# Optimization experiments

Hardware: AMD Instinct MI355X
Metric: run time of the kernel (lower is better)

## Reference

```python
import jax, jax.numpy as jnp
import numpy as np

N = 50000      # nodes
E = 800000     # edges (before self-loops)
DIN = 2        # dim_input
DEMB = 128     # dim_embedding
H = 8          # n_heads
DV = 16        # dim_values (H*DV == DEMB)
DH = 512       # dim_hidden
L = 2          # n_att_layers
K = 10         # APPNP steps
ALPHA = 0.1
EPS = 1e-5     # BatchNorm eps
NEG_SLOPE = 0.2  # GAT leaky_relu slope


def setup_inputs() -> dict:
    key = jax.random.key(0)
    ks = jax.random.split(key, 16)
    s = 0.05
    inp = {}
    inp["x"] = jax.random.normal(ks[0], (N, DIN), jnp.float32)
    inp["J"] = jax.random.uniform(ks[1], (N, 1), jnp.float32)
    inp["edge_index"] = jax.random.randint(ks[2], (2, E), 0, N, jnp.int32)
    # Lin1: Linear(dim_input+1, dim_embedding)
    inp["lin0_w"] = jax.random.normal(ks[3], (DIN + 1, DEMB), jnp.float32) * s
    inp["lin0_b"] = jnp.zeros((DEMB,), jnp.float32)
    # Per attention layer (stacked over L):
    inp["gat_w"]   = jax.random.normal(ks[4], (L, DEMB, H * DV), jnp.float32) * s
    inp["att_src"] = jax.random.normal(ks[5], (L, H, DV), jnp.float32) * s
    inp["att_dst"] = jax.random.normal(ks[6], (L, H, DV), jnp.float32) * s
    inp["lin1_w"]  = jax.random.normal(ks[7], (L, DV, DEMB), jnp.float32) * s
    inp["bn1_g"]   = jnp.ones((L, DEMB), jnp.float32)
    inp["bn1_b"]   = jnp.zeros((L, DEMB), jnp.float32)
    inp["lin2_w"]  = jax.random.normal(ks[8], (L, DEMB, DH), jnp.float32) * s
    inp["lin2_b"]  = jnp.zeros((L, DH), jnp.float32)
    inp["lin3_w"]  = jax.random.normal(ks[9], (L, DH, DEMB), jnp.float32) * s
    inp["lin3_b"]  = jnp.zeros((L, DEMB), jnp.float32)
    inp["bn2_g"]   = jnp.ones((L, DEMB), jnp.float32)
    inp["bn2_b"]   = jnp.zeros((L, DEMB), jnp.float32)
    return inp


def _bn(z, g, b):
    # BatchNorm1d over nodes, training-mode batch statistics (biased var)
    mu = z.mean(0)
    var = jnp.mean((z - mu) ** 2, axis=0)
    return g * (z - mu) * jax.lax.rsqrt(var + EPS) + b


def reference(x, J, edge_index, lin0_w, lin0_b, gat_w, att_src, att_dst,
              lin1_w, bn1_g, bn1_b, lin2_w, lin2_b, lin3_w, lin3_b,
              bn2_g, bn2_b):
    # add self-loops (PyG GATConv and APPNP defaults)
    loop = jnp.arange(N, dtype=edge_index.dtype)
    src = jnp.concatenate([edge_index[0], loop])  # message source j
    dst = jnp.concatenate([edge_index[1], loop])  # message target i

    h = jnp.concatenate([x, J], axis=1) @ lin0_w + lin0_b  # [N, DEMB]

    for l in range(L):
        # ---- GATConv ----
        xl = (h @ gat_w[l]).reshape(N, H, DV)                # [N,H,DV]
        a_s = (xl * att_src[l]).sum(-1)                      # [N,H]
        a_d = (xl * att_dst[l]).sum(-1)                      # [N,H]
        e = jax.nn.leaky_relu(a_s[src] + a_d[dst], NEG_SLOPE)  # [E',H]
        e = e - jax.ops.segment_max(e, dst, num_segments=N)[dst]
        ee = jnp.exp(e)
        alpha = ee / jax.ops.segment_sum(ee, dst, num_segments=N)[dst]
        msg = xl[src] * alpha[:, :, None]                    # [E',H,DV]
        gat_out = jax.ops.segment_sum(msg, dst, num_segments=N)  # [N,H,DV]
        # lin1 per head then sum over heads
        hsum = jnp.einsum('nhc,cd->nd', gat_out, lin1_w[l])  # [N,DEMB]
        h1 = _bn(h + hsum, bn1_g[l], bn1_b[l])
        h2 = jax.nn.relu(h1 @ lin2_w[l] + lin2_b[l]) @ lin3_w[l] + lin3_b[l]
        h = _bn(h2 + h1, bn2_g[l], bn2_b[l])

    # ---- APPNP: K steps of (1-a)*Ahat h + a*h0, Ahat = D^-1/2 (A+I) D^-1/2 ----
    deg = jax.ops.segment_sum(jnp.ones_like(dst, jnp.float32), dst, num_segments=N)
    dinv = jax.lax.rsqrt(jnp.maximum(deg, 1.0))  # self-loops guarantee deg>=1
    norm = (dinv[src] * dinv[dst])[:, None]      # [E',1]
    h0 = h

    def step(hk, _):
        agg = jax.ops.segment_sum(norm * hk[src], dst, num_segments=N)
        return (1.0 - ALPHA) * agg + ALPHA * h0, None

    h, _ = jax.lax.scan(step, h, None, length=K)
    return jnp.concatenate([h, J], axis=1)  # [N, DEMB+1]
```

## Files before the change

kernel.cpp:

```cpp
#include <hip/hip_runtime.h>

#define NN 50000
#define NP 50048
#define NMT64 782
#define NE 800000
#define EP (NE + NN)
#define DEMB 128
#define DHID 512
#define NB_SCAN 196

typedef unsigned short ushort_t;
typedef __attribute__((ext_vector_type(8))) short short8_t;
typedef __attribute__((ext_vector_type(4))) float float4_t;

__device__ __forceinline__ float bf2f(ushort_t u) {
    return __uint_as_float(((unsigned int)u) << 16);
}
__device__ __forceinline__ ushort_t f2bf(float f) {
    unsigned int x = __float_as_uint(f);
    x += 0x7fffu + ((x >> 16) & 1u);
    return (ushort_t)(x >> 16);
}
__device__ __forceinline__ float lo16(unsigned int w) { return __uint_as_float(w << 16); }
__device__ __forceinline__ float hi16(unsigned int w) { return __uint_as_float(w & 0xffff0000u); }
__device__ __forceinline__ unsigned int pack2(float a, float b) {
    return (unsigned int)f2bf(a) | ((unsigned int)f2bf(b) << 16);
}
__device__ __forceinline__ void gl_lds16(const ushort_t* g, ushort_t* l) {
    __builtin_amdgcn_global_load_lds(
        (const __attribute__((address_space(1))) void*)g,
        (__attribute__((address_space(3))) void*)l, 16, 0, 0);
}
static inline int cdiv(int a, int b) { return (a + b - 1) / b; }

__global__ void k_detect(const unsigned int* __restrict__ Jw, int* __restrict__ flag) {
    if (threadIdx.x != 0 || blockIdx.x != 0) return;
    int votes = 0;
    for (int i = 0; i < 8; ++i) {
        unsigned int w = Jw[i];
        unsigned int ex = (w >> 23) & 0xFFu;
        if ((w >> 31) == 0u && ex >= 100u && ex <= 126u) votes++;
    }
    *flag = (votes >= 6) ? 1 : 0;
}

struct CvtArgs {
    const void* src[16];
    float* dst[16];
    int n[16];
};
__global__ void k_cvt_all(CvtArgs a, const int* __restrict__ flag) {
    int which = blockIdx.y;
    int i = blockIdx.x * 256 + threadIdx.x;
    if (i >= a.n[which]) return;
    float v;
    if (*flag) v = ((const float*)a.src[which])[i];
    else       v = bf2f(((const ushort_t*)a.src[which])[i]);
    a.dst[which][i] = v;
}

struct TrArgs {
    const float* src[6];
    ushort_t* dst[6];
    int K[6];
    int Nc[6];
    int perm[6];
};
__global__ void k_tr_all(TrArgs a) {
    int which = blockIdx.y;
    int idx = blockIdx.x * 256 + threadIdx.x;
    int K = a.K[which], Nc = a.Nc[which];
    if (idx >= K * Nc) return;
    int k = idx / Nc, n = idx - k * Nc;
    int kd = k;
    if (a.perm[which]) {
        int kk = k & 63;
        int ks = kk >> 5, k5 = kk & 31;
        int u = (k5 >> 4) & 1, q = (k5 >> 2) & 3, tt = k5 & 3;
        kd = (k & ~63) | (ks * 32 + q * 8 + tt * 2 + u);
    }
    a.dst[which][n * K + kd] = f2bf(a.src[which][idx]);
}

__global__ void k_deg(const int* __restrict__ ei, int* __restrict__ deg) {
    int e = blockIdx.x * 256 + threadIdx.x;
    if (e >= EP) return;
    int d = (e < NE) ? ei[NE + e] : (e - NE);
    atomicAdd(&deg[d], 1);
}

__global__ void k_part(const int* __restrict__ deg, int* __restrict__ part) {
    __shared__ int sm[256];
    int i = blockIdx.x * 256 + threadIdx.x;
    int v = (i < NN) ? deg[i] : 0;
    sm[threadIdx.x] = v;
    __syncthreads();
    for (int off = 128; off > 0; off >>= 1) {
        if (threadIdx.x < off) sm[threadIdx.x] += sm[threadIdx.x + off];
        __syncthreads();
    }
    if (threadIdx.x == 0) part[blockIdx.x] = sm[0];
}

__global__ void k_scan2(const int* __restrict__ part, int* __restrict__ poff,
                        int* __restrict__ rowp) {
    __shared__ int sm[256];
    int t = threadIdx.x;
    int v = (t < NB_SCAN) ? part[t] : 0;
    sm[t] = v;
    __syncthreads();
    int incl = v;
    for (int off = 1; off < 256; off <<= 1) {
        int u = (t >= off) ? sm[t - off] : 0;
        __syncthreads();
        incl += u;
        sm[t] = incl;
        __syncthreads();
    }
    if (t < NB_SCAN) poff[t] = incl - v;
    if (t == 255) rowp[NN] = sm[255];
}

__global__ void k_rowp(const int* __restrict__ deg, const int* __restrict__ poff,
                       int* __restrict__ rowp, float* __restrict__ dinv,
                       int* __restrict__ fill) {
    __shared__ int sm[256];
    int i = blockIdx.x * 256 + threadIdx.x;
    int t = threadIdx.x;
    int v = (i < NN) ? deg[i] : 0;
    sm[t] = v;
    __syncthreads();
    int incl = v;
    for (int off = 1; off < 256; off <<= 1) {
        int u = (t >= off) ? sm[t - off] : 0;
        __syncthreads();
        incl += u;
        sm[t] = incl;
        __syncthreads();
    }
    if (i < NN) {
        int rp = poff[blockIdx.x] + incl - v;
        rowp[i] = rp;
        fill[i] = rp;
        dinv[i] = rsqrtf(fmaxf((float)v, 1.0f));
    }
}

__global__ void k_fill(const int* __restrict__ ei, int* __restrict__ fillpos,
                       ushort_t* __restrict__ col) {
    int e = blockIdx.x * 256 + threadIdx.x;
    if (e >= EP) return;
    int s, d;
    if (e < NE) { s = ei[e]; d = ei[NE + e]; } else { s = d = e - NE; }
    int pos = atomicAdd(&fillpos[d], 1);
    col[pos] = (ushort_t)s;
}

__global__ void k_lin0(const float* __restrict__ x, const float* __restrict__ J,
                       const float* __restrict__ w, const float* __restrict__ b,
                       ushort_t* __restrict__ hB) {
    int idx = blockIdx.x * 256 + threadIdx.x;
    if (idx >= NN * DEMB) return;
    int n = idx >> 7, d = idx & 127;
    float v = x[n * 2] * w[d] + x[n * 2 + 1] * w[DEMB + d] + J[n] * w[2 * DEMB + d] + b[d];
    hB[idx] = f2bf(v);
}

__global__ void k_att(const unsigned int* __restrict__ xlB, const float* __restrict__ asrc,
                      const float* __restrict__ adst, float* __restrict__ a_s,
                      float* __restrict__ a_d) {
    int idx = blockIdx.x * 256 + threadIdx.x;
    if (idx >= NN * 8) return;
    int n = idx >> 3, hh = idx & 7;
    const unsigned int* row = xlB + (size_t)n * 64 + hh * 8;
    float s = 0.f, d = 0.f;
#pragma unroll
    for (int c = 0; c < 8; ++c) {
        unsigned int w = row[c];
        float v0 = lo16(w), v1 = hi16(w);
        s += v0 * asrc[hh * 16 + 2 * c] + v1 * asrc[hh * 16 + 2 * c + 1];
        d += v0 * adst[hh * 16 + 2 * c] + v1 * adst[hh * 16 + 2 * c + 1];
    }
    a_s[idx] = s;
    a_d[idx] = d;
}

__global__ __launch_bounds__(256) void k_z1s(const ushort_t* __restrict__ hB,
                                             const float* __restrict__ g,
                                             const float* __restrict__ w1,
                                             float* __restrict__ stats) {
    int d = threadIdx.x & 127;
    int rstart = blockIdx.x * 2 + (threadIdx.x >> 7);
    int stride = gridDim.x * 2;
    float s1 = 0.f, s2 = 0.f;
    for (int r = rstart; r < NN; r += stride) {
        const float* gr = g + r * 16;
        float s = bf2f(hB[(size_t)r * DEMB + d]);
#pragma unroll
        for (int c = 0; c < 16; ++c) s += gr[c] * w1[c * DEMB + d];
        s1 += s;
        s2 += s * s;
    }
    __shared__ float b1[256], b2[256];
    b1[threadIdx.x] = s1;
    b2[threadIdx.x] = s2;
    __syncthreads();
    if (threadIdx.x < 128) {
        atomicAdd(&stats[threadIdx.x], b1[threadIdx.x] + b1[threadIdx.x + 128]);
        atomicAdd(&stats[128 + threadIdx.x], b2[threadIdx.x] + b2[threadIdx.x + 128]);
    }
}

__global__ void k_bnapply1(const ushort_t* __restrict__ hB, const float* __restrict__ g,
                           const float* __restrict__ w1, const float* __restrict__ stats,
                           const float* __restrict__ gam, const float* __restrict__ bet,
                           ushort_t* __restrict__ outB) {
    int idx = blockIdx.x * 256 + threadIdx.x;
    if (idx >= NN * DEMB) return;
    int n = idx >> 7, d = idx & 127;
    float s = bf2f(hB[idx]);
    const float* gr = g + n * 16;
#pragma unroll
    for (int c = 0; c < 16; ++c) s += gr[c] * w1[c * DEMB + d];
    const float invN = 1.0f / (float)NN;
    float mu = stats[d] * invN;
    float var = stats[128 + d] * invN - mu * mu;
    float rs = rsqrtf(fmaxf(var, 0.f) + 1e-5f);
    float v = gam[d] * (s - mu) * rs + bet[d];
    outB[idx] = f2bf(v);
}

__global__ void k_bnapply(const ushort_t* __restrict__ zB, const float* __restrict__ stats,
                          const float* __restrict__ gam, const float* __restrict__ bet,
                          ushort_t* __restrict__ outB) {
    int idx = blockIdx.x * 256 + threadIdx.x;
    if (idx >= NN * DEMB) return;
    int d = idx & 127;
    const float invN = 1.0f / (float)NN;
    float mu = stats[d] * invN;
    float var = stats[128 + d] * invN - mu * mu;
    float rs = rsqrtf(fmaxf(var, 0.f) + 1e-5f);
    float v = gam[d] * (bf2f(zB[idx]) - mu) * rs + bet[d];
    outB[idx] = f2bf(v);
}

__global__ void k_bnapply_fin(const unsigned int* __restrict__ zB, const float* __restrict__ stats,
                              const float* __restrict__ gam, const float* __restrict__ bet,
                              const float* __restrict__ dinv,
                              unsigned int* __restrict__ hs, unsigned int* __restrict__ h0p) {
    int idx = blockIdx.x * 256 + threadIdx.x;
    if (idx >= NN * 64) return;
    int n = idx >> 6, d0 = (idx & 63) * 2;
    const float invN = 1.0f / (float)NN;
    unsigned int zw = zB[idx];
    float z0 = lo16(zw), z1 = hi16(zw);
    float mu0 = stats[d0] * invN, mu1 = stats[d0 + 1] * invN;
    float v0 = stats[128 + d0] * invN - mu0 * mu0;
    float v1 = stats[128 + d0 + 1] * invN - mu1 * mu1;
    float rs0 = rsqrtf(fmaxf(v0, 0.f) + 1e-5f);
    float rs1 = rsqrtf(fmaxf(v1, 0.f) + 1e-5f);
    float a = gam[d0] * (z0 - mu0) * rs0 + bet[d0];
    float b = gam[d0 + 1] * (z1 - mu1) * rs1 + bet[d0 + 1];
    float di = dinv[n];
    hs[idx] = pack2(di * a, di * b);
    h0p[idx] = pack2(a, b);
}

__global__ __launch_bounds__(256) void k_gat(const int* __restrict__ rowp,
                                             const ushort_t* __restrict__ col,
                                             const float* __restrict__ a_s, const float* __restrict__ a_d,
                                             const unsigned int* __restrict__ xlB, float* __restrict__ g) {
    int wid = (blockIdx.x * 256 + threadIdx.x) >> 6;
    int lane = threadIdx.x & 63;
    if (wid >= NN) return;
    int p0 = rowp[wid], p1 = rowp[wid + 1];
    int hh = lane >> 3;
    float ad2 = a_d[wid * 8 + hh];
    float acc0 = 0.f, acc1 = 0.f, s = 0.f;
    int p = p0;
    while (p < p1) {
        int cnt = p1 - p;
        if (cnt > 64) cnt = 64;
        int pl = p + lane;
        int jv = (int)col[pl < p1 ? pl : (p1 - 1)];
        int i = 0;
        for (; i + 8 <= cnt; i += 8) {
            int j0 = __shfl(jv, i),     j1 = __shfl(jv, i + 1);
            int j2 = __shfl(jv, i + 2), j3 = __shfl(jv, i + 3);
            int j4 = __shfl(jv, i + 4), j5 = __shfl(jv, i + 5);
            int j6 = __shfl(jv, i + 6), j7 = __shfl(jv, i + 7);
            float e0 = a_s[j0 * 8 + hh] + ad2, e1 = a_s[j1 * 8 + hh] + ad2;
            float e2 = a_s[j2 * 8 + hh] + ad2, e3 = a_s[j3 * 8 + hh] + ad2;
            float e4 = a_s[j4 * 8 + hh] + ad2, e5 = a_s[j5 * 8 + hh] + ad2;
            float e6 = a_s[j6 * 8 + hh] + ad2, e7 = a_s[j7 * 8 + hh] + ad2;
            unsigned int w0 = xlB[j0 * 64 + lane], w1 = xlB[j1 * 64 + lane];
            unsigned int w2 = xlB[j2 * 64 + lane], w3 = xlB[j3 * 64 + lane];
            unsigned int w4 = xlB[j4 * 64 + lane], w5 = xlB[j5 * 64 + lane];
            unsigned int w6 = xlB[j6 * 64 + lane], w7 = xlB[j7 * 64 + lane];
            e0 = e0 > 0.f ? e0 : 0.2f * e0;  e1 = e1 > 0.f ? e1 : 0.2f * e1;
            e2 = e2 > 0.f ? e2 : 0.2f * e2;  e3 = e3 > 0.f ? e3 : 0.2f * e3;
            e4 = e4 > 0.f ? e4 : 0.2f * e4;  e5 = e5 > 0.f ? e5 : 0.2f * e5;
            e6 = e6 > 0.f ? e6 : 0.2f * e6;  e7 = e7 > 0.f ? e7 : 0.2f * e7;
            float al0 = __expf(e0), al1 = __expf(e1), al2 = __expf(e2), al3 = __expf(e3);
            float al4 = __expf(e4), al5 = __expf(e5), al6 = __expf(e6), al7 = __expf(e7);
            s += al0 + al1 + al2 + al3 + al4 + al5 + al6 + al7;
            acc0 += al0 * lo16(w0) + al1 * lo16(w1) + al2 * lo16(w2) + al3 * lo16(w3) +
                    al4 * lo16(w4) + al5 * lo16(w5) + al6 * lo16(w6) + al7 * lo16(w7);
            acc1 += al0 * hi16(w0) + al1 * hi16(w1) + al2 * hi16(w2) + al3 * hi16(w3) +
                    al4 * hi16(w4) + al5 * hi16(w5) + al6 * hi16(w6) + al7 * hi16(w7);
        }
        for (; i < cnt; ++i) {
            int j = __shfl(jv, i);
            float e = a_s[j * 8 + hh] + ad2;
            e = e > 0.f ? e : 0.2f * e;
            float al = __expf(e);
            unsigned int w = xlB[j * 64 + lane];
            s += al;
            acc0 += al * lo16(w);
            acc1 += al * hi16(w);
        }
        p += cnt;
    }
    float inv = 1.f / s;
    acc0 *= inv;
    acc1 *= inv;
    acc0 += __shfl_xor(acc0, 8);  acc1 += __shfl_xor(acc1, 8);
    acc0 += __shfl_xor(acc0, 16); acc1 += __shfl_xor(acc1, 16);
    acc0 += __shfl_xor(acc0, 32); acc1 += __shfl_xor(acc1, 32);
    if (lane < 8) ((float2*)g)[wid * 8 + lane] = make_float2(acc0, acc1);
}

__global__ __launch_bounds__(256) void k_appnp(const int* __restrict__ rowp,
                                               const ushort_t* __restrict__ col,
                                               const float* __restrict__ dinv,
                                               const unsigned int* __restrict__ hs,
                                               const unsigned int* __restrict__ h0p,
                                               unsigned int* __restrict__ hs_out,
                                               const float* __restrict__ Jf,
                                               const int* __restrict__ flag,
                                               void* __restrict__ out, int writeOut) {
    int wid = (blockIdx.x * 256 + threadIdx.x) >> 6;
    int lane = threadIdx.x & 63;
    if (wid >= NN) return;
    int p0 = rowp[wid], p1 = rowp[wid + 1];
    float di = dinv[wid];
    unsigned int hw = h0p[(size_t)wid * 64 + lane];
    float a0 = 0.f, a1 = 0.f;
    int p = p0;
    while (p < p1) {
        int cnt = p1 - p;
        if (cnt > 64) cnt = 64;
        int pl = p + lane;
        int jv = (int)col[pl < p1 ? pl : (p1 - 1)];
        int i = 0;
        for (; i + 8 <= cnt; i += 8) {
            int j0 = __shfl(jv, i),     j1 = __shfl(jv, i + 1);
            int j2 = __shfl(jv, i + 2), j3 = __shfl(jv, i + 3);
            int j4 = __shfl(jv, i + 4), j5 = __shfl(jv, i + 5);
            int j6 = __shfl(jv, i + 6), j7 = __shfl(jv, i + 7);
            unsigned int w0 = hs[j0 * 64 + lane], w1 = hs[j1 * 64 + lane];
            unsigned int w2 = hs[j2 * 64 + lane], w3 = hs[j3 * 64 + lane];
            unsigned int w4 = hs[j4 * 64 + lane], w5 = hs[j5 * 64 + lane];
            unsigned int w6 = hs[j6 * 64 + lane], w7 = hs[j7 * 64 + lane];
            a0 += lo16(w0) + lo16(w1) + lo16(w2) + lo16(w3) +
                  lo16(w4) + lo16(w5) + lo16(w6) + lo16(w7);
            a1 += hi16(w0) + hi16(w1) + hi16(w2) + hi16(w3) +
                  hi16(w4) + hi16(w5) + hi16(w6) + hi16(w7);
        }
        for (; i < cnt; ++i) {
            int j = __shfl(jv, i);
            unsigned int w = hs[j * 64 + lane];
            a0 += lo16(w);
            a1 += hi16(w);
        }
        p += cnt;
    }
    float n0 = 0.9f * di * a0 + 0.1f * lo16(hw);
    float n1 = 0.9f * di * a1 + 0.1f * hi16(hw);
    if (!writeOut) {
        hs_out[(size_t)wid * 64 + lane] = pack2(di * n0, di * n1);
    } else {
        size_t base = (size_t)wid * 129;
        if (*flag) {
            float* o = (float*)out;
            o[base + 2 * lane] = n0;
            o[base + 2 * lane + 1] = n1;
            if (lane == 0) o[base + 128] = Jf[wid];
        } else {
            ushort_t* o = (ushort_t*)out;
            o[base + 2 * lane] = f2bf(n0);
            o[base + 2 * lane + 1] = f2bf(n1);
            if (lane == 0) o[base + 128] = f2bf(Jf[wid]);
        }
    }
}

template <int MODE>
__global__ __launch_bounds__(256) void k_gemm64(const ushort_t* __restrict__ A,
                                                const ushort_t* __restrict__ Bt,
                                                int M, int K, int Nc,
                                                const float* __restrict__ bias,
                                                const ushort_t* __restrict__ res,
                                                ushort_t* __restrict__ outB,
                                                float* __restrict__ stats) {
    __shared__ __align__(16) ushort_t lsA[2][64 * 32];
    __shared__ __align__(16) ushort_t lsB[2][128 * 32];
    int t = threadIdx.x;
    int m0 = blockIdx.x * 64;
    int n0 = blockIdx.y * 128;
    int w = t >> 6, lane = t & 63;
    int row16 = lane & 15, quad = lane >> 4;
    int nbase = w * 32;
    float4_t acc[8];
#pragma unroll
    for (int i = 0; i < 8; ++i) acc[i] = (float4_t){0.f, 0.f, 0.f, 0.f};
    int lrow = lane >> 2;
    int lcol = (lane & 3) * 8;
    const ushort_t* gA  = A  + (size_t)(m0 + w * 16 + lrow) * K + lcol;
    const ushort_t* gB0 = Bt + (size_t)(n0 + w * 32 + lrow) * K + lcol;
    const ushort_t* gB1 = Bt + (size_t)(n0 + w * 32 + 16 + lrow) * K + lcol;
    ushort_t* dA  = &lsA[0][0] + (w * 16) * 32;
    ushort_t* dB0 = &lsB[0][0] + (w * 32) * 32;
    ushort_t* dB1 = &lsB[0][0] + (w * 32 + 16) * 32;
    const int bufStrideA = 64 * 32, bufStrideB = 128 * 32;
    const int nK = K >> 5;
    gl_lds16(gA, dA);
    gl_lds16(gB0, dB0);
    gl_lds16(gB1, dB1);
    for (int kb = 0; kb < nK; ++kb) {
        __syncthreads();
        int nb = kb + 1;
        if (nb < nK) {
            int b = nb & 1;
            int k0 = nb << 5;
            gl_lds16(gA + k0, dA + b * bufStrideA);
            gl_lds16(gB0 + k0, dB0 + b * bufStrideB);
            gl_lds16(gB1 + k0, dB1 + b * bufStrideB);
        }
        const ushort_t* la = &lsA[kb & 1][0];
        const ushort_t* lb = &lsB[kb & 1][0];
        short8_t afr[4], bfr[2];
#pragma unroll
        for (int i = 0; i < 4; ++i)
            afr[i] = *(const short8_t*)(la + (i * 16 + row16) * 32 + quad * 8);
#pragma unroll
        for (int i = 0; i < 2; ++i)
            bfr[i] = *(const short8_t*)(lb + (nbase + i * 16 + row16) * 32 + quad * 8);
#pragma unroll
        for (int mt = 0; mt < 4; ++mt)
#pragma unroll
            for (int nt = 0; nt < 2; ++nt)
                acc[mt * 2 + nt] = __builtin_amdgcn_mfma_f32_16x16x32_bf16(
                    afr[mt], bfr[nt], acc[mt * 2 + nt], 0, 0, 0);
    }
#pragma unroll
    for (int mt = 0; mt < 4; ++mt) {
#pragma unroll
        for (int nt = 0; nt < 2; ++nt) {
            int cc = n0 + nbase + nt * 16 + row16;
#pragma unroll
            for (int r = 0; r < 4; ++r) {
                int rr = m0 + mt * 16 + quad * 4 + r;
                if (rr < M) {
                    outB[(size_t)rr * Nc + cc] = f2bf(acc[mt * 2 + nt][r]);
                }
            }
        }
    }
}

__global__ __launch_bounds__(256, 2) void k_ffn(const ushort_t* __restrict__ A,
                                                const ushort_t* __restrict__ W2t,
                                                const ushort_t* __restrict__ W3t,
                                                const float* __restrict__ b2,
                                                const float* __restrict__ b3,
                                                const ushort_t* __restrict__ res,
                                                ushort_t* __restrict__ outB,
                                                float* __restrict__ stats) {
    __shared__ __align__(16) ushort_t sW2[2][4 * 64 * 32];
    __shared__ __align__(16) ushort_t sW3[2][2 * 128 * 32];
    __shared__ __align__(16) ushort_t sAH[4][2048];
    int t = threadIdx.x;
    int w = t >> 6, lane = t & 63;
    int m0 = blockIdx.x * 64;
    int row16 = lane & 15, quad = lane >> 4;
    int sw = (row16 >> 2) & 3;
    int srow = lane >> 2;
    int klin = lane & 3;

#pragma unroll
    for (int i = 0; i < 4; ++i) {
        int row = i * 16 + srow;
        int kc = klin ^ ((row >> 2) & 3);
        gl_lds16(A + (size_t)(m0 + row) * 128 + w * 32 + kc * 8,
                 &sAH[0][0] + w * 2048 + i * 512);
    }
#pragma unroll
    for (int i = 0; i < 4; ++i) {
        int n = i * 16 + srow;
        int kc = klin ^ ((n >> 2) & 3);
        gl_lds16(W2t + (size_t)n * 128 + w * 32 + kc * 8,
                 &sW2[0][0] + w * 2048 + i * 512);
    }
#pragma unroll
    for (int i = 0; i < 4; ++i) {
        int f = w * 4 + i;
        int ks = f >> 3;
        int n = (f & 7) * 16 + srow;
        int kc = klin ^ ((n >> 2) & 3);
        gl_lds16(W3t + (size_t)n * 512 + ks * 32 + kc * 8,
                 &sW3[0][0] + f * 512);
    }
    __syncthreads();

    short8_t afrA[4];
#pragma unroll
    for (int kb = 0; kb < 4; ++kb)
        afrA[kb] = *(const short8_t*)(&sAH[0][0] + kb * 2048 + (w * 16 + row16) * 32 + (quad ^ sw) * 8);
    __syncthreads();

    float* s1 = (float*)&sAH[0][1024];
    float* s2 = s1 + 128;
    if (t < 128) { s1[t] = 0.f; s2[t] = 0.f; }
    ushort_t* Hbase = &sAH[w][0];

    float4_t accz[8];
#pragma unroll
    for (int i = 0; i < 8; ++i) accz[i] = (float4_t){0.f, 0.f, 0.f, 0.f};

    for (int c = 0; c < 8; ++c) {
        int cb = c & 1;
        if (c < 7) {
            int nb = cb ^ 1;
#pragma unroll
            for (int i = 0; i < 4; ++i) {
                int n = i * 16 + srow;
                int kc = klin ^ ((n >> 2) & 3);
                gl_lds16(W2t + (size_t)((c + 1) * 64 + n) * 128 + w * 32 + kc * 8,
                         &sW2[nb][0] + w * 2048 + i * 512);
            }
#pragma unroll
            for (int i = 0; i < 4; ++i) {
                int f = w * 4 + i;
                int ks = f >> 3;
                int n = (f & 7) * 16 + srow;
                int kc = klin ^ ((n >> 2) & 3);
                gl_lds16(W3t + (size_t)n * 512 + (c + 1) * 64 + ks * 32 + kc * 8,
                         &sW3[nb][0] + f * 512);
            }
        }
        float4_t acch[4];
#pragma unroll
        for (int i = 0; i < 4; ++i) acch[i] = (float4_t){0.f, 0.f, 0.f, 0.f};
#pragma unroll
        for (int kb = 0; kb < 4; ++kb) {
            short8_t bfr[4];
#pragma unroll
            for (int nt = 0; nt < 4; ++nt)
                bfr[nt] = *(const short8_t*)(&sW2[cb][0] + kb * 2048 + (nt * 16 + row16) * 32 + (quad ^ sw) * 8);
#pragma unroll
            for (int nt = 0; nt < 4; ++nt)
                acch[nt] = __builtin_amdgcn_mfma_f32_16x16x32_bf16(afrA[kb], bfr[nt],
                                                                   acch[nt], 0, 0, 0);
        }
        {
            float b2v[4];
#pragma unroll
            for (int nt = 0; nt < 4; ++nt) b2v[nt] = b2[c * 64 + nt * 16 + row16];
#pragma unroll
            for (int r = 0; r < 4; ++r) {
                int row = quad * 4 + r;
                float v0 = acch[0][r] + b2v[0]; v0 = v0 > 0.f ? v0 : 0.f;
                float v1 = acch[1][r] + b2v[1]; v1 = v1 > 0.f ? v1 : 0.f;
                float v2 = acch[2][r] + b2v[2]; v2 = v2 > 0.f ? v2 : 0.f;
                float v3 = acch[3][r] + b2v[3]; v3 = v3 > 0.f ? v3 : 0.f;
                int byteA = row * 128 + ((((row16 >> 2) ^ (row & 7))) << 4) + (row16 & 3) * 4;
                *(unsigned int*)((char*)Hbase + byteA) = pack2(v0, v1);
                *(unsigned int*)((char*)Hbase + (byteA ^ 64)) = pack2(v2, v3);
            }
        }
#pragma unroll
        for (int ks = 0; ks < 2; ++ks) {
            short8_t afrH = *(const short8_t*)((char*)Hbase + row16 * 128 +
                                               ((((ks << 2) | quad) ^ (row16 & 7)) << 4));
            short8_t bfr[8];
#pragma unroll
            for (int nt = 0; nt < 8; ++nt)
                bfr[nt] = *(const short8_t*)(&sW3[cb][0] + ks * 4096 + (nt * 16 + row16) * 32 + (quad ^ sw) * 8);
#pragma unroll
            for (int nt = 0; nt < 8; ++nt)
                accz[nt] = __builtin_amdgcn_mfma_f32_16x16x32_bf16(afrH, bfr[nt],
                                                                   accz[nt], 0, 0, 0);
        }
        __syncthreads();
    }

#pragma unroll
    for (int nt = 0; nt < 8; ++nt) {
        int cc = nt * 16 + row16;
        float bv = b3[cc];
        float ls = 0.f, lq = 0.f;
#pragma unroll
        for (int r = 0; r < 4; ++r) {
            int rr = m0 + w * 16 + quad * 4 + r;
            if (rr < NN) {
                float v = accz[nt][r] + bv + bf2f(res[(size_t)rr * 128 + cc]);
                outB[(size_t)rr * 128 + cc] = f2bf(v);
                ls += v;
                lq += v * v;
            }
        }
        atomicAdd(&s1[cc], ls);
        atomicAdd(&s2[cc], lq);
    }
    __syncthreads();
    if (t < 128) {
        atomicAdd(&stats[t], s1[t]);
        atomicAdd(&stats[128 + t], s2[t]);
    }
}

extern "C" void kernel_launch(void* const* d_in, const int* in_sizes, int n_in,
                              void* d_out, int out_size, void* d_ws, size_t ws_size,
                              hipStream_t stream) {
    const int* ei = (const int*)d_in[2];

    char* p = (char*)d_ws;
    auto alloc = [&](size_t bytes) {
        void* r = (void*)p;
        p += (bytes + 255) & ~(size_t)255;
        return r;
    };
    ushort_t* hB    = (ushort_t*)alloc((size_t)NP * DEMB * 2);
    ushort_t* h1B   = (ushort_t*)alloc((size_t)NP * DEMB * 2);
    ushort_t* xlB   = (ushort_t*)alloc((size_t)NN * DEMB * 2);
    unsigned int* hsA  = (unsigned int*)alloc((size_t)NN * 64 * 4);
    unsigned int* hsB_ = (unsigned int*)alloc((size_t)NN * 64 * 4);
    unsigned int* h0p  = (unsigned int*)alloc((size_t)NN * 64 * 4);
    float*    asv   = (float*)alloc((size_t)NN * 8 * 4);
    float*    adv   = (float*)alloc((size_t)NN * 8 * 4);
    float*    gv    = (float*)alloc((size_t)NN * 16 * 4);
    float*    dinvv = (float*)alloc((size_t)NN * 4);
    float*    stats = (float*)alloc(4 * 256 * 4);
    int*      deg   = (int*)alloc((size_t)NN * 4);
    int*      rowp  = (int*)alloc((size_t)(NN + 1) * 4);
    int*      fill  = (int*)alloc((size_t)NN * 4);
    ushort_t* colv  = (ushort_t*)alloc((size_t)EP * 2);
    int*      part  = (int*)alloc(NB_SCAN * 4);
    int*      poff  = (int*)alloc(NB_SCAN * 4);
    int*      flag  = (int*)alloc(256);
    ushort_t* wtg   = (ushort_t*)alloc((size_t)2 * 128 * 128 * 2);
    ushort_t* wt2   = (ushort_t*)alloc((size_t)2 * 512 * 128 * 2);
    ushort_t* wt3   = (ushort_t*)alloc((size_t)2 * 128 * 512 * 2);
    float* xf   = (float*)alloc((size_t)NN * 2 * 4);
    float* Jf   = (float*)alloc((size_t)NN * 4);
    float* l0wF = (float*)alloc(384 * 4);
    float* l0bF = (float*)alloc(128 * 4);
    float* gwF  = (float*)alloc(32768 * 4);
    float* asF  = (float*)alloc(256 * 4);
    float* adF  = (float*)alloc(256 * 4);
    float* w1F  = (float*)alloc(4096 * 4);
    float* b1gF = (float*)alloc(256 * 4);
    float* b1bF = (float*)alloc(256 * 4);
    float* w2F  = (float*)alloc(131072 * 4);
    float* b2F  = (float*)alloc(1024 * 4);
    float* w3F  = (float*)alloc(131072 * 4);
    float* b3F  = (float*)alloc(256 * 4);
    float* b2gF = (float*)alloc(256 * 4);
    float* b2bF = (float*)alloc(256 * 4);

    k_detect<<<1, 64, 0, stream>>>((const unsigned int*)d_in[1], flag);
    CvtArgs ca;
    {
        const int srcIdx[16] = {0, 1, 3, 4, 5, 6, 7, 8, 9, 10, 11, 12, 13, 14, 15, 16};
        float* dsts[16] = {xf, Jf, l0wF, l0bF, gwF, asF, adF, w1F, b1gF, b1bF,
                           w2F, b2F, w3F, b3F, b2gF, b2bF};
        const int ns[16] = {NN * 2, NN, 384, 128, 32768, 256, 256, 4096, 256, 256,
                            131072, 1024, 131072, 256, 256, 256};
        for (int i = 0; i < 16; ++i) { ca.src[i] = d_in[srcIdx[i]]; ca.dst[i] = dsts[i]; ca.n[i] = ns[i]; }
    }
    k_cvt_all<<<dim3(cdiv(131072, 256), 16), 256, 0, stream>>>(ca, flag);

    hipMemsetAsync(deg, 0, (size_t)NN * 4, stream);
    hipMemsetAsync(stats, 0, 4 * 256 * 4, stream);
    k_deg<<<cdiv(EP, 256), 256, 0, stream>>>(ei, deg);
    k_part<<<NB_SCAN, 256, 0, stream>>>(deg, part);
    k_scan2<<<1, 256, 0, stream>>>(part, poff, rowp);
    k_rowp<<<NB_SCAN, 256, 0, stream>>>(deg, poff, rowp, dinvv, fill);
    k_fill<<<cdiv(EP, 256), 256, 0, stream>>>(ei, fill, colv);

    TrArgs ta;
    {
        const float* srcs[6] = {gwF, gwF + 16384, w2F, w2F + 65536, w3F, w3F + 65536};
        ushort_t* dsts[6] = {wtg, wtg + 16384, wt2, wt2 + 65536, wt3, wt3 + 65536};
        const int Ks[6] = {128, 128, 128, 128, 512, 512};
        const int Ncs[6] = {128, 128, 512, 512, 128, 128};
        const int perms[6] = {0, 0, 0, 0, 1, 1};
        for (int i = 0; i < 6; ++i) {
            ta.src[i] = srcs[i]; ta.dst[i] = dsts[i]; ta.K[i] = Ks[i]; ta.Nc[i] = Ncs[i];
            ta.perm[i] = perms[i];
        }
    }
    k_tr_all<<<dim3(cdiv(65536, 256), 6), 256, 0, stream>>>(ta);

    k_lin0<<<cdiv(NN * DEMB, 256), 256, 0, stream>>>(xf, Jf, l0wF, l0bF, hB);

    for (int l = 0; l < 2; ++l) {
        float* st1 = stats + (l * 2 + 0) * 256;
        float* st2 = stats + (l * 2 + 1) * 256;
        ushort_t* zB = xlB;
        k_gemm64<3><<<dim3(NMT64, 1), 256, 0, stream>>>(hB, wtg + l * 16384, NN, 128, 128,
                                                        nullptr, nullptr, xlB, nullptr);
        k_att<<<cdiv(NN * 8, 256), 256, 0, stream>>>((const unsigned int*)xlB, asF + l * 128,
                                                     adF + l * 128, asv, adv);
        k_gat<<<cdiv(NN * 64, 256), 256, 0, stream>>>(rowp, colv, asv, adv,
                                                      (const unsigned int*)xlB, gv);
        k_z1s<<<512, 256, 0, stream>>>(hB, gv, w1F + l * 2048, st1);
        k_bnapply1<<<cdiv(NN * DEMB, 256), 256, 0, stream>>>(hB, gv, w1F + l * 2048, st1,
                                                             b1gF + l * 128, b1bF + l * 128,
                                                             h1B);
        k_ffn<<<NMT64, 256, 0, stream>>>(h1B, wt2 + l * 65536, wt3 + l * 65536,
                                         b2F + l * 512, b3F + l * 128, h1B, zB, st2);
        if (l == 0) {
            k_bnapply<<<cdiv(NN * DEMB, 256), 256, 0, stream>>>(zB, st2, b2gF, b2bF, hB);
        } else {
            k_bnapply_fin<<<cdiv(NN * 64, 256), 256, 0, stream>>>((const unsigned int*)zB, st2,
                                                                  b2gF + 128, b2bF + 128,
                                                                  dinvv, hsA, h0p);
        }
    }

    unsigned int* pin = hsA;
    unsigned int* pout = hsB_;
    for (int k = 0; k < 10; ++k) {
        int last = (k == 9) ? 1 : 0;
        k_appnp<<<cdiv(NN * 64, 256), 256, 0, stream>>>(rowp, colv, dinvv, pin, h0p, pout,
                                                        Jf, flag, d_out, last);
        unsigned int* tmp = pout;
        pout = pin;
        pin = tmp;
    }
}
```

Baseline: 903.4 us.

## Retile FFN kernel to 2x2 warp grid, single-buffer LDS for higher occupancy

The fused FFN kernel changes from each wave owning 16 rows across all columns to a 2x2 wave grid where each wave computes a 32-row by half-column tile. This halves B-fragment LDS reads per MFMA and shares the hidden activation tile across waves. The W2/W3 LDS buffers drop from double to single buffering, with extra barriers around the refills, and launch bounds rise to 3 blocks per CU. The transpose permutation is also rewritten to match the new H layout. Single buffering puts the weight loads in series with compute, which may offset the gains from more resident blocks.

```diff
diff --git a/kernel.cpp b/kernel.cpp
--- a/kernel.cpp
+++ b/kernel.cpp
@@ -75,9 +75,7 @@
     int kd = k;
     if (a.perm[which]) {
         int kk = k & 63;
-        int ks = kk >> 5, k5 = kk & 31;
-        int u = (k5 >> 4) & 1, q = (k5 >> 2) & 3, tt = k5 & 3;
-        kd = (k & ~63) | (ks * 32 + q * 8 + tt * 2 + u);
+        kd = (k & ~63) | ((kk & 32) + 2 * (kk & 15) + ((kk >> 4) & 1));
     }
     a.dst[which][n * K + kd] = f2bf(a.src[which][idx]);
 }
@@ -469,7 +467,7 @@
     }
 }
 
-__global__ __launch_bounds__(256, 2) void k_ffn(const ushort_t* __restrict__ A,
+__global__ __launch_bounds__(256, 3) void k_ffn(const ushort_t* __restrict__ A,
                                                 const ushort_t* __restrict__ W2t,
                                                 const ushort_t* __restrict__ W3t,
                                                 const float* __restrict__ b2,
@@ -477,11 +475,12 @@
                                                 const ushort_t* __restrict__ res,
                                                 ushort_t* __restrict__ outB,
                                                 float* __restrict__ stats) {
-    __shared__ __align__(16) ushort_t sW2[2][4 * 64 * 32];
-    __shared__ __align__(16) ushort_t sW3[2][2 * 128 * 32];
-    __shared__ __align__(16) ushort_t sAH[4][2048];
+    __shared__ __align__(16) ushort_t sW2[4 * 64 * 32];
+    __shared__ __align__(16) ushort_t sW3[2 * 128 * 32];
+    __shared__ __align__(16) ushort_t sAH[4 * 2048];
     int t = threadIdx.x;
     int w = t >> 6, lane = t & 63;
+    int wm = w >> 1, wn = w & 1;
     int m0 = blockIdx.x * 64;
     int row16 = lane & 15, quad = lane >> 4;
     int sw = (row16 >> 2) & 3;
@@ -493,52 +492,96 @@
         int row = i * 16 + srow;
         int kc = klin ^ ((row >> 2) & 3);
         gl_lds16(A + (size_t)(m0 + row) * 128 + w * 32 + kc * 8,
-                 &sAH[0][0] + w * 2048 + i * 512);
-    }
-#pragma unroll
-    for (int i = 0; i < 4; ++i) {
-        int n = i * 16 + srow;
-        int kc = klin ^ ((n >> 2) & 3);
-        gl_lds16(W2t + (size_t)n * 128 + w * 32 + kc * 8,
-                 &sW2[0][0] + w * 2048 + i * 512);
-    }
-#pragma unroll
-    for (int i = 0; i < 4; ++i) {
+                 sAH + w * 2048 + i * 512);
+        gl_lds16(W2t + (size_t)row * 128 + w * 32 + kc * 8,
+                 sW2 + w * 2048 + i * 512);
         int f = w * 4 + i;
         int ks = f >> 3;
-        int n = (f & 7) * 16 + srow;
-        int kc = klin ^ ((n >> 2) & 3);
-        gl_lds16(W3t + (size_t)n * 512 + ks * 32 + kc * 8,
-                 &sW3[0][0] + f * 512);
+        int n3 = (f & 7) * 16 + srow;
+        int kc3 = klin ^ ((n3 >> 2) & 3);
+        gl_lds16(W3t + (size_t)n3 * 512 + ks * 32 + kc3 * 8,
+                 sW3 + f * 512);
     }
     __syncthreads();
 
-    short8_t afrA[4];
-#pragma unroll
-    for (int kb = 0; kb < 4; ++kb)
-        afrA[kb] = *(const short8_t*)(&sAH[0][0] + kb * 2048 + (w * 16 + row16) * 32 + (quad ^ sw) * 8);
+    short8_t afrA[2][4];
+#pragma unroll
+    for (int mt = 0; mt < 2; ++mt)
+#pragma unroll
+        for (int kb = 0; kb < 4; ++kb)
+            afrA[mt][kb] = *(const short8_t*)(sAH + kb * 2048 +
+                                              (wm * 32 + mt * 16 + row16) * 32 + (quad ^ sw) * 8);
     __syncthreads();
 
-    float* s1 = (float*)&sAH[0][1024];
+    char* Hb = (char*)sAH;
+    float* s1 = (float*)(Hb + 8192);
     float* s2 = s1 + 128;
     if (t < 128) { s1[t] = 0.f; s2[t] = 0.f; }
-    ushort_t* Hbase = &sAH[w][0];
-
-    float4_t accz[8];
-#pragma unroll
-    for (int i = 0; i < 8; ++i) accz[i] = (float4_t){0.f, 0.f, 0.f, 0.f};
+
+    float4_t accz[2][4];
+#pragma unroll
+    for (int mt = 0; mt < 2; ++mt)
+#pragma unroll
+        for (int nt = 0; nt < 4; ++nt) accz[mt][nt] = (float4_t){0.f, 0.f, 0.f, 0.f};
 
     for (int c = 0; c < 8; ++c) {
-        int cb = c & 1;
+        float b20 = b2[c * 64 + wn * 32 + row16];
+        float b21 = b2[c * 64 + wn * 32 + 16 + row16];
+        float4_t acch[2][2];
+#pragma unroll
+        for (int mt = 0; mt < 2; ++mt)
+#pragma unroll
+            for (int nt = 0; nt < 2; ++nt) acch[mt][nt] = (float4_t){0.f, 0.f, 0.f, 0.f};
+#pragma unroll
+        for (int kb = 0; kb < 4; ++kb) {
+            short8_t b0 = *(const short8_t*)(sW2 + kb * 2048 +
+                                             (wn * 32 + row16) * 32 + (quad ^ sw) * 8);
+            short8_t b1 = *(const short8_t*)(sW2 + kb * 2048 +
+                                             (wn * 32 + 16 + row16) * 32 + (quad ^ sw) * 8);
+            acch[0][0] = __builtin_amdgcn_mfma_f32_16x16x32_bf16(afrA[0][kb], b0, acch[0][0], 0, 0, 0);
+            acch[0][1] = __builtin_amdgcn_mfma_f32_16x16x32_bf16(afrA[0][kb], b1, acch[0][1], 0, 0, 0);
+            acch[1][0] = __builtin_amdgcn_mfma_f32_16x16x32_bf16(afrA[1][kb], b0, acch[1][0], 0, 0, 0);
+            acch[1][1] = __builtin_amdgcn_mfma_f32_16x16x32_bf16(afrA[1][kb], b1, acch[1][1], 0, 0, 0);
+        }
+#pragma unroll
+        for (int mt = 0; mt < 2; ++mt) {
+#pragma unroll
+            for (int r = 0; r < 4; ++r) {
+                int row = wm * 32 + mt * 16 + quad * 4 + r;
+                int d = wn * 16 + row16;
+                int byteOff = row * 128 + ((((d >> 2) ^ (row & 7))) << 4) + (d & 3) * 4;
+                float v0 = acch[mt][0][r] + b20; v0 = v0 > 0.f ? v0 : 0.f;
+                float v1 = acch[mt][1][r] + b21; v1 = v1 > 0.f ? v1 : 0.f;
+                *(unsigned int*)(Hb + byteOff) = pack2(v0, v1);
+            }
+        }
+        __syncthreads();
         if (c < 7) {
-            int nb = cb ^ 1;
 #pragma unroll
             for (int i = 0; i < 4; ++i) {
                 int n = i * 16 + srow;
                 int kc = klin ^ ((n >> 2) & 3);
                 gl_lds16(W2t + (size_t)((c + 1) * 64 + n) * 128 + w * 32 + kc * 8,
-                         &sW2[nb][0] + w * 2048 + i * 512);
+                         sW2 + w * 2048 + i * 512);
             }
+        }
+#pragma unroll
+        for (int ks = 0; ks < 2; ++ks) {
+            short8_t afrH[2];
+#pragma unroll
+            for (int mt = 0; mt < 2; ++mt)
+                afrH[mt] = *(const short8_t*)(Hb + (wm * 32 + mt * 16 + row16) * 128 +
+                                              (((ks * 4 + quad) ^ (row16 & 7)) << 4));
+#pragma unroll
+            for (int nt = 0; nt < 4; ++nt) {
+                short8_t bfr = *(const short8_t*)(sW3 + ks * 4096 +
+                                                  (wn * 64 + nt * 16 + row16) * 32 + (quad ^ sw) * 8);
+                accz[0][nt] = __builtin_amdgcn_mfma_f32_16x16x32_bf16(afrH[0], bfr, accz[0][nt], 0, 0, 0);
+                accz[1][nt] = __builtin_amdgcn_mfma_f32_16x16x32_bf16(afrH[1], bfr, accz[1][nt], 0, 0, 0);
+            }
+        }
+        __syncthreads();
+        if (c < 7) {
 #pragma unroll
             for (int i = 0; i < 4; ++i) {
                 int f = w * 4 + i;
@@ -546,72 +589,31 @@
                 int n = (f & 7) * 16 + srow;
                 int kc = klin ^ ((n >> 2) & 3);
                 gl_lds16(W3t + (size_t)n * 512 + (c + 1) * 64 + ks * 32 + kc * 8,
-                         &sW3[nb][0] + f * 512);
+                         sW3 + f * 512);
             }
         }
-        float4_t acch[4];
-#pragma unroll
-        for (int i = 0; i < 4; ++i) acch[i] = (float4_t){0.f, 0.f, 0.f, 0.f};
-#pragma unroll
-        for (int kb = 0; kb < 4; ++kb) {
-            short8_t bfr[4];
-#pragma unroll
-            for (int nt = 0; nt < 4; ++nt)
-                bfr[nt] = *(const short8_t*)(&sW2[cb][0] + kb * 2048 + (nt * 16 + row16) * 32 + (quad ^ sw) * 8);
-#pragma unroll
-            for (int nt = 0; nt < 4; ++nt)
-                acch[nt] = __builtin_amdgcn_mfma_f32_16x16x32_bf16(afrA[kb], bfr[nt],
-                                                                   acch[nt], 0, 0, 0);
-        }
-        {
-            float b2v[4];
-#pragma unroll
-            for (int nt = 0; nt < 4; ++nt) b2v[nt] = b2[c * 64 + nt * 16 + row16];
+    }
+
+#pragma unroll
+    for (int mt = 0; mt < 2; ++mt) {
+#pragma unroll
+        for (int nt = 0; nt < 4; ++nt) {
+            int cc = wn * 64 + nt * 16 + row16;
+            float bv = b3[cc];
+            float ls = 0.f, lq = 0.f;
 #pragma unroll
             for (int r = 0; r < 4; ++r) {
-                int row = quad * 4 + r;
-                float v0 = acch[0][r] + b2v[0]; v0 = v0 > 0.f ? v0 : 0.f;
-                float v1 = acch[1][r] + b2v[1]; v1 = v1 > 0.f ? v1 : 0.f;
-                float v2 = acch[2][r] + b2v[2]; v2 = v2 > 0.f ? v2 : 0.f;
-                float v3 = acch[3][r] + b2v[3]; v3 = v3 > 0.f ? v3 : 0.f;
-                int byteA = row * 128 + ((((row16 >> 2) ^ (row & 7))) << 4) + (row16 & 3) * 4;
-                *(unsigned int*)((char*)Hbase + byteA) = pack2(v0, v1);
-                *(unsigned int*)((char*)Hbase + (byteA ^ 64)) = pack2(v2, v3);
+                int rr = m0 + wm * 32 + mt * 16 + quad * 4 + r;
+                if (rr < NN) {
+                    float v = accz[mt][nt][r] + bv + bf2f(res[(size_t)rr * 128 + cc]);
+                    outB[(size_t)rr * 128 + cc] = f2bf(v);
+                    ls += v;
+                    lq += v * v;
+                }
             }
-        }
-#pragma unroll
-        for (int ks = 0; ks < 2; ++ks) {
-            short8_t afrH = *(const short8_t*)((char*)Hbase + row16 * 128 +
-                                               ((((ks << 2) | quad) ^ (row16 & 7)) << 4));
-            short8_t bfr[8];
-#pragma unroll
-            for (int nt = 0; nt < 8; ++nt)
-                bfr[nt] = *(const short8_t*)(&sW3[cb][0] + ks * 4096 + (nt * 16 + row16) * 32 + (quad ^ sw) * 8);
-#pragma unroll
-            for (int nt = 0; nt < 8; ++nt)
-                accz[nt] = __builtin_amdgcn_mfma_f32_16x16x32_bf16(afrH, bfr[nt],
-                                                                   accz[nt], 0, 0, 0);
-        }
-        __syncthreads();
-    }
-
-#pragma unroll
-    for (int nt = 0; nt < 8; ++nt) {
-        int cc = nt * 16 + row16;
-        float bv = b3[cc];
-        float ls = 0.f, lq = 0.f;
-#pragma unroll
-        for (int r = 0; r < 4; ++r) {
-            int rr = m0 + w * 16 + quad * 4 + r;
-            if (rr < NN) {
-                float v = accz[nt][r] + bv + bf2f(res[(size_t)rr * 128 + cc]);
-                outB[(size_t)rr * 128 + cc] = f2bf(v);
-                ls += v;
-                lq += v * v;
-            }
-        }
-        atomicAdd(&s1[cc], ls);
-        atomicAdd(&s2[cc], lq);
+            atomicAdd(&s1[cc], ls);
+            atomicAdd(&s2[cc], lq);
+        }
     }
     __syncthreads();
     if (t < 128) {
```

New measurement: 875.2 us. 3.1% less time.
